# Optimization experiments

Hardware: AMD Instinct MI355X
Metric: run time of the kernel (lower is better)

Reference implementation:

```python
import jax, jax.numpy as jnp
import numpy as np

FREQ_DIM = 32
TIME_DIM = 32
HEADS = 8
TWO_PI = 6.283185307179586


def get_embeddings(B, H, W, freq_dim, time_dim, dtype):
    # freq embeddings over the height (frequency) axis
    nf = freq_dim // 2
    ln_x = jnp.log2(jnp.arange(0, H * nf, dtype=jnp.float32))
    ln_x = ln_x.at[0].set(-2.0)
    ln_x = ln_x.reshape(H, nf).T  # [nf, H]
    ln_x = ln_x * jnp.arange(1, nf + 1, dtype=jnp.float32)[:, None]
    # view_as_real(exp(1j*theta)) -> (cos, sin), interleaved per order along channel dim
    freq = jnp.stack([jnp.cos(ln_x), jnp.sin(ln_x)], axis=1).reshape(freq_dim, H)  # [freq_dim, H]
    freq = jnp.broadcast_to(freq[None, :, :, None], (B, freq_dim, H, W))

    # time embeddings over the width (time) axis
    nt = time_dim // 2
    k = jnp.arange(0, nt, dtype=jnp.float32) + 0.5  # [nt]
    x = jnp.arange(0, nt * W, dtype=jnp.float32).reshape(W, nt).T  # [nt, W]
    theta = k[:, None] * x / (W * nt) * TWO_PI  # [nt, W]
    time = jnp.stack([jnp.cos(theta), jnp.sin(theta)], axis=1).reshape(time_dim, W)  # [time_dim, W]
    time = jnp.broadcast_to(time[None, :, None, :], (B, time_dim, H, W))

    return jnp.concatenate([freq, time], axis=1).astype(dtype)  # [B, freq_dim+time_dim, H, W]


def setup_inputs() -> dict:
    key = jax.random.key(0)
    ks = jax.random.split(key, 6)
    B, C, H, W = 2, 512, 64, 32
    qkC = C + FREQ_DIM + TIME_DIM  # 576
    inner = HEADS * 64  # 512
    return {
        "hidden_states": jax.random.normal(ks[0], (B, C, H, W), dtype=jnp.float32),
        "Wq": jax.random.normal(ks[1], (qkC, inner), dtype=jnp.float32) * 0.02,
        "Wk": jax.random.normal(ks[2], (qkC, inner), dtype=jnp.float32) * 0.02,
        "Wv": jax.random.normal(ks[3], (C, inner), dtype=jnp.float32) * 0.02,
        "Wout": jax.random.normal(ks[4], (inner, C), dtype=jnp.float32) * 0.02,
        "bout": jnp.zeros((C,), dtype=jnp.float32),
    }


def reference(hidden_states, Wq, Wk, Wv, Wout, bout):
    B, C, H, W = hidden_states.shape
    emb = get_embeddings(B, H, W, FREQ_DIM, TIME_DIM, hidden_states.dtype)
    qk_hs = jnp.concatenate([hidden_states, emb], axis=1)  # [B, qkC, H, W]

    S = H * W
    qk_hs = qk_hs.reshape(B, -1, S).transpose(0, 2, 1)  # [B, S, qkC]
    v_hs = hidden_states.reshape(B, C, S).transpose(0, 2, 1)  # [B, S, C]

    q = qk_hs @ Wq  # [B, S, inner]
    k = qk_hs @ Wk
    v = v_hs @ Wv

    hd_qk = q.shape[-1] // HEADS
    hd_v = v.shape[-1] // HEADS
    q = q.reshape(B, S, HEADS, hd_qk).transpose(0, 2, 1, 3)  # [B, h, S, d]
    k = k.reshape(B, S, HEADS, hd_qk).transpose(0, 2, 1, 3)
    v = v.reshape(B, S, HEADS, hd_v).transpose(0, 2, 1, 3)

    scale = 1.0 / jnp.sqrt(jnp.asarray(hd_qk, dtype=q.dtype))
    scores = jnp.einsum('bhqd,bhkd->bhqk', q, k) * scale
    attn = jax.nn.softmax(scores, axis=-1)
    o = jnp.einsum('bhqk,bhkd->bhqd', attn, v)  # [B, h, S, d_v]

    o = o.transpose(0, 2, 1, 3).reshape(B, S, HEADS * hd_v)
    o = o @ Wout + bout  # [B, S, C]
    o = o.transpose(0, 2, 1).reshape(B, C, H, W)

    return o + hidden_states  # residual_connection=True, rescale_output_factor=1.0
```

## Files before the change

kernel.cpp:

```cpp
#include <hip/hip_runtime.h>
#include <math.h>

#define B_    2
#define C_    512
#define H_    64
#define W_    32
#define S_    2048
#define QKC_  576
#define INNER_ 512
#define NH_   8
#define HD_   64
#define TWO_PI_ 6.283185307179586f

typedef __attribute__((ext_vector_type(8))) short bfrag;
typedef __attribute__((ext_vector_type(4))) float ffrag;
typedef __attribute__((ext_vector_type(16))) float f16v;

typedef __attribute__((address_space(1))) const unsigned int as1_u32;
typedef __attribute__((address_space(3))) unsigned int as3_u32;

__device__ __forceinline__ ushort f2bf(float f) {
    unsigned u = __builtin_bit_cast(unsigned, f);
    unsigned r = (u + 0x7FFFu + ((u >> 16) & 1u)) >> 16;
    return (ushort)r;
}

__device__ __forceinline__ f16v zero16() {
    f16v z;
    #pragma unroll
    for (int i = 0; i < 16; i++) z[i] = 0.f;
    return z;
}

#define GLD(gp_, lp_) __builtin_amdgcn_global_load_lds((as1_u32*)(gp_), (as3_u32*)(lp_), 16, 0, 0)
#define EXPA(dst_, x_) asm("v_exp_f32 %0, %1" : "=v"(dst_) : "v"(x_))
#define SC_LOG2E 0.18033688011f

__global__ void k_trans_emb(const float* __restrict__ hid, ushort* __restrict__ X) {
    __shared__ float t[32][33];
    int b  = blockIdx.z;
    int s0 = blockIdx.x * 32, c0 = blockIdx.y * 32;
    int tx = threadIdx.x, ty = threadIdx.y;
    if (c0 < 512) {
        t[ty][tx] = hid[((size_t)b * C_ + (c0 + ty)) * S_ + s0 + tx];
        __syncthreads();
        X[((size_t)(b * S_ + s0 + ty)) * QKC_ + c0 + tx] = f2bf(t[tx][ty]);
    } else {
        int c = c0 - 512 + tx;
        int s = s0 + ty;
        int h = s >> 5, w = s & 31;
        float val;
        if (c < 32) {
            int f = c >> 1;
            int n = h * 16 + f;
            float lx = (n == 0) ? -2.0f : log2f((float)n);
            float arg = lx * (float)(f + 1);
            val = (c & 1) ? sinf(arg) : cosf(arg);
        } else {
            int tt = (c - 32) >> 1;
            float theta = ((float)tt + 0.5f) * (float)(w * 16 + tt) * (TWO_PI_ / 512.0f);
            val = (c & 1) ? sinf(theta) : cosf(theta);
        }
        X[(size_t)(b * S_ + s) * QKC_ + c0 + tx] = f2bf(val);
    }
}

__global__ void k_wtrans_all(const float* __restrict__ Wq, const float* __restrict__ Wk,
                             const float* __restrict__ Wv, const float* __restrict__ Wo,
                             ushort* __restrict__ Wqt, ushort* __restrict__ Wkt,
                             ushort* __restrict__ Wvt, ushort* __restrict__ Wot) {
    __shared__ float t[32][33];
    int z = blockIdx.z;
    const float* W; ushort* Wt; int K;
    if (z == 0)      { W = Wq; Wt = Wqt; K = QKC_; }
    else if (z == 1) { W = Wk; Wt = Wkt; K = QKC_; }
    else if (z == 2) { W = Wv; Wt = Wvt; K = C_; }
    else             { W = Wo; Wt = Wot; K = INNER_; }
    int k0 = blockIdx.x * 32, n0 = blockIdx.y * 32;
    if (k0 >= K) return;
    int tx = threadIdx.x, ty = threadIdx.y;
    t[ty][tx] = W[(size_t)(k0 + ty) * 512 + n0 + tx];
    __syncthreads();
    Wt[(size_t)(n0 + ty) * K + k0 + tx] = f2bf(t[tx][ty]);
}

#define GSTAGE(buf_, k0_) {                                                   \
    _Pragma("unroll")                                                         \
    for (int i_ = 0; i_ < 6; i_++)                                            \
        GLD(gp[i_] + (k0_), tl + (buf_) * 12288 + lo[i_]); }

__global__ __launch_bounds__(256, 3) void k_qkv(const ushort* __restrict__ X,
                                                const ushort* __restrict__ Wqt,
                                                const ushort* __restrict__ Wkt,
                                                const ushort* __restrict__ Wvt,
                                                ushort* __restrict__ Qb,
                                                ushort* __restrict__ Kpk,
                                                ushort* __restrict__ Vpk) {
    __shared__ ushort __attribute__((aligned(16))) tl[2 * 12288];

    int tid = threadIdx.x;
    int l = tid & 63, wv = tid >> 6;
    int wr = wv >> 1, wc = wv & 1;
    int bid = blockIdx.x;
    int lgc = (bid & 7) * 96 + (bid >> 3);
    int bx = lgc % 24, by = lgc / 24;
    int n0 = bx * 64, m0 = by * 128;
    int sel = n0 >> 9, n0l = n0 & 511;
    const ushort* Bt = (sel == 0) ? Wqt : (sel == 1) ? Wkt : Wvt;
    const int K = (sel < 2) ? QKC_ : C_;
    const int nst = K >> 6;
    int l15 = l & 15, lg = l >> 4;
    int swz = l15 & 7;

    const ushort* gp[6];
    unsigned lo[6];
    {
        int rsub = l >> 3;
        int clog = (l & 7) ^ rsub;
        #pragma unroll
        for (int i = 0; i < 6; i++) {
            int c = wv * 6 + i;
            lo[i] = c * 512;
            if (c < 16) gp[i] = X  + (size_t)(m0  + c * 8        + rsub) * QKC_ + clog * 8;
            else        gp[i] = Bt + (size_t)(n0l + (c - 16) * 8 + rsub) * K    + clog * 8;
        }
    }

    ffrag acc[4][2];
    #pragma unroll
    for (int i = 0; i < 4; i++)
        #pragma unroll
        for (int j = 0; j < 2; j++) acc[i][j] = (ffrag){0.f, 0.f, 0.f, 0.f};

    GSTAGE(0, 0);
    int cur = 0;
    for (int kt = 0; kt < nst; kt++) {
        __syncthreads();
        if (kt + 1 < nst) GSTAGE(cur ^ 1, (kt + 1) * 64);
        const ushort* As = tl + cur * 12288;
        const ushort* Bs = As + 8192;
        #pragma unroll
        for (int ks = 0; ks < 2; ks++) {
            int cl = ks * 4 + lg;
            int ch = (cl ^ swz) * 8;
            bfrag af[4], bf[2];
            #pragma unroll
            for (int mi = 0; mi < 4; mi++)
                af[mi] = *(const bfrag*)(As + (wr * 64 + mi * 16 + l15) * 64 + ch);
            #pragma unroll
            for (int nj = 0; nj < 2; nj++)
                bf[nj] = *(const bfrag*)(Bs + (wc * 32 + nj * 16 + l15) * 64 + ch);
            #pragma unroll
            for (int mi = 0; mi < 4; mi++)
                #pragma unroll
                for (int nj = 0; nj < 2; nj++)
                    acc[mi][nj] = __builtin_amdgcn_mfma_f32_16x16x32_bf16(af[mi], bf[nj], acc[mi][nj], 0, 0, 0);
        }
        cur ^= 1;
    }

    if (sel == 0) {
        #pragma unroll
        for (int mi = 0; mi < 4; mi++)
            #pragma unroll
            for (int nj = 0; nj < 2; nj++)
                #pragma unroll
                for (int r = 0; r < 4; r++) {
                    int row = m0 + wr * 64 + mi * 16 + lg * 4 + r;
                    int col = n0l + wc * 32 + nj * 16 + l15;
                    Qb[(size_t)row * INNER_ + col] = f2bf(acc[mi][nj][r] * SC_LOG2E);
                }
    } else {
        ushort (*Ct)[136] = (ushort(*)[136])tl;
        __syncthreads();
        #pragma unroll
        for (int mi = 0; mi < 4; mi++)
            #pragma unroll
            for (int nj = 0; nj < 2; nj++)
                #pragma unroll
                for (int r = 0; r < 4; r++)
                    Ct[wc * 32 + nj * 16 + l15][wr * 64 + mi * 16 + lg * 4 + r] = f2bf(acc[mi][nj][r]);
        __syncthreads();
        int pair = (m0 >> 11) * 8 + (n0l >> 6);
        int kvb0 = (m0 & 2047) >> 5;
        if (sel == 1) {
            #pragma unroll
            for (int p = 0; p < 4; p++) {
                int cid = tid + p * 256;
                int sl = cid >> 7, kv = cid & 127;
                bfrag tmp;
                #pragma unroll
                for (int j = 0; j < 8; j++) tmp[j] = (short)Ct[sl * 8 + j][kv];
                ushort* dst = Kpk + ((size_t)((pair * 64 + kvb0 + (kv >> 5)) * 8 + sl)) * 256 + (kv & 31) * 8;
                *(uint4*)dst = __builtin_bit_cast(uint4, tmp);
            }
        } else {
            #pragma unroll
            for (int p = 0; p < 4; p++) {
                int cid = tid + p * 256;
                int d = cid >> 4, mc = cid & 15;
                uint4 v = *(uint4*)&Ct[d][mc * 8];
                ushort* dst = Vpk + ((size_t)((pair * 64 + kvb0 + (mc >> 2)) * 4 + (mc & 3))) * 512 + d * 8;
                *(uint4*)dst = v;
            }
        }
    }
}

__global__ __launch_bounds__(256, 2) void k_og(const ushort* __restrict__ Ob,
                                               const ushort* __restrict__ Wot,
                                               const float* __restrict__ bias,
                                               const float* __restrict__ hid,
                                               float* __restrict__ out) {
    __shared__ ushort __attribute__((aligned(16))) tl[2 * 12288];

    int tid = threadIdx.x;
    int l = tid & 63, wv = tid >> 6;
    int wr = wv >> 1, wc = wv & 1;
    int bid = blockIdx.x;
    int lgc = (bid & 7) * 32 + (bid >> 3);
    int bx = lgc & 7, by = lgc >> 3;
    int n0 = bx * 64, m0 = by * 128;
    int l15 = l & 15, lg = l >> 4;
    int swz = l15 & 7;

    const ushort* gp[6];
    unsigned lo[6];
    {
        int rsub = l >> 3;
        int clog = (l & 7) ^ rsub;
        #pragma unroll
        for (int i = 0; i < 6; i++) {
            int c = wv * 6 + i;
            lo[i] = c * 512;
            if (c < 16) gp[i] = Ob  + (size_t)(m0 + c * 8        + rsub) * INNER_ + clog * 8;
            else        gp[i] = Wot + (size_t)(n0 + (c - 16) * 8 + rsub) * INNER_ + clog * 8;
        }
    }

    ffrag acc[4][2];
    #pragma unroll
    for (int i = 0; i < 4; i++)
        #pragma unroll
        for (int j = 0; j < 2; j++) acc[i][j] = (ffrag){0.f, 0.f, 0.f, 0.f};

    GSTAGE(0, 0);
    int cur = 0;
    for (int kt = 0; kt < 8; kt++) {
        __syncthreads();
        if (kt < 7) GSTAGE(cur ^ 1, (kt + 1) * 64);
        const ushort* As = tl + cur * 12288;
        const ushort* Bs = As + 8192;
        #pragma unroll
        for (int ks = 0; ks < 2; ks++) {
            int cl = ks * 4 + lg;
            int ch = (cl ^ swz) * 8;
            bfrag af[4], bf[2];
            #pragma unroll
            for (int mi = 0; mi < 4; mi++)
                af[mi] = *(const bfrag*)(As + (wr * 64 + mi * 16 + l15) * 64 + ch);
            #pragma unroll
            for (int nj = 0; nj < 2; nj++)
                bf[nj] = *(const bfrag*)(Bs + (wc * 32 + nj * 16 + l15) * 64 + ch);
            #pragma unroll
            for (int mi = 0; mi < 4; mi++)
                #pragma unroll
                for (int nj = 0; nj < 2; nj++)
                    acc[mi][nj] = __builtin_amdgcn_mfma_f32_16x16x32_bf16(af[mi], bf[nj], acc[mi][nj], 0, 0, 0);
        }
        cur ^= 1;
    }

    float (*Cf)[129] = (float(*)[129])tl;
    float bv[2];
    #pragma unroll
    for (int nj = 0; nj < 2; nj++) bv[nj] = bias[n0 + wc * 32 + nj * 16 + l15];
    __syncthreads();
    #pragma unroll
    for (int mi = 0; mi < 4; mi++)
        #pragma unroll
        for (int nj = 0; nj < 2; nj++)
            #pragma unroll
            for (int r = 0; r < 4; r++)
                Cf[wc * 32 + nj * 16 + l15][wr * 64 + mi * 16 + lg * 4 + r] = acc[mi][nj][r] + bv[nj];
    __syncthreads();
    int b = m0 >> 11, s0m = m0 & 2047;
    #pragma unroll
    for (int p = 0; p < 8; p++) {
        int f = p * 256 + tid;
        int c = f >> 5, sq = (f & 31) * 4;
        size_t o = (((size_t)(b * 512 + n0 + c)) << 11) + s0m + sq;
        float4 hv = *(const float4*)(hid + o);
        float4 cv = *(float4*)&Cf[c][sq];
        cv.x += hv.x; cv.y += hv.y; cv.z += hv.z; cv.w += hv.w;
        *(float4*)(out + o) = cv;
    }
}

#define CVTPK(dst, a, b) asm("v_cvt_pk_bf16_f32 %0, %1, %2" : "=v"(dst) : "v"(a), "v"(b))
#define SWAP32(a, b)     asm("v_permlane32_swap_b32 %0, %1" : "+v"(a), "+v"(b))

#define KLOAD(dst_, kt_) {                                                    \
    const ushort* g_ = kpb + (size_t)(kt_) * 2048 + kro;                      \
    _Pragma("unroll")                                                         \
    for (int ks_ = 0; ks_ < 4; ks_++) dst_[ks_] = *(const bfrag*)(g_ + ks_ * 512); }

#define VLOAD(dst_, kt_) {                                                    \
    const ushort* g_ = vpb + (size_t)(kt_) * 2048 + vro;                      \
    dst_[0] = *(const bfrag*)(g_);                                            \
    dst_[1] = *(const bfrag*)(g_ + 256);                                      \
    dst_[2] = *(const bfrag*)(g_ + 1024);                                     \
    dst_[3] = *(const bfrag*)(g_ + 1280); }

#define PVHALF(sf_, vf_, a0_, a1_) {                                          \
    _Pragma("unroll")                                                         \
    for (int s = 0; s < 2; s++) {                                             \
        unsigned A0, B0, A1, B1;                                              \
        CVTPK(A0, sf_[s * 8 + 0], sf_[s * 8 + 1]); CVTPK(B0, sf_[s * 8 + 4], sf_[s * 8 + 5]); \
        SWAP32(A0, B0);                                                       \
        CVTPK(A1, sf_[s * 8 + 2], sf_[s * 8 + 3]); CVTPK(B1, sf_[s * 8 + 6], sf_[s * 8 + 7]); \
        SWAP32(A1, B1);                                                       \
        uint4 u_; u_.x = A0; u_.y = A1; u_.z = B0; u_.w = B1;                 \
        bfrag pa_ = __builtin_bit_cast(bfrag, u_);                            \
        a0_ = __builtin_amdgcn_mfma_f32_32x32x16_bf16(vf_[s * 2],     pa_, a0_, 0, 0, 0); \
        a1_ = __builtin_amdgcn_mfma_f32_32x32x16_bf16(vf_[s * 2 + 1], pa_, a1_, 0, 0, 0); \
    } }

#define ABODY(kf_, vf_) {                                                     \
    f16v sfA = zero16(), sfB = zero16();                                      \
    __builtin_amdgcn_s_setprio(1);                                            \
    _Pragma("unroll")                                                         \
    for (int ks = 0; ks < 4; ks++) {                                          \
        sfA = __builtin_amdgcn_mfma_f32_32x32x16_bf16(kf_[ks], qfA[ks], sfA, 0, 0, 0); \
        sfB = __builtin_amdgcn_mfma_f32_32x32x16_bf16(kf_[ks], qfB[ks], sfB, 0, 0, 0); \
    }                                                                         \
    __builtin_amdgcn_s_setprio(0);                                            \
    float lsA = 0.f, lsB = 0.f;                                               \
    _Pragma("unroll")                                                         \
    for (int j = 0; j < 16; j++) {                                            \
        float pA; EXPA(pA, sfA[j]); sfA[j] = pA; lsA += pA;                   \
        float pB; EXPA(pB, sfB[j]); sfB[j] = pB; lsB += pB;                   \
    }                                                                         \
    lA += lsA; lB += lsB;                                                     \
    __builtin_amdgcn_s_setprio(1);                                            \
    PVHALF(sfA, vf_, accA0, accA1);                                           \
    PVHALF(sfB, vf_, accB0, accB1);                                           \
    __builtin_amdgcn_s_setprio(0); }

__global__ __launch_bounds__(512, 2) void k_attn(const ushort* __restrict__ Qf,
                                                 const ushort* __restrict__ Kpk,
                                                 const ushort* __restrict__ Vpk,
                                                 ushort* __restrict__ Ob) {
    __shared__ __attribute__((aligned(16))) char smem[35840];
    float* cmb = (float*)smem;
    float* lsh = (float*)(smem + 33792);

    const int id  = blockIdx.x;
    const int xcd = id & 7, wi = id >> 3;
    const int pair = xcd * 2 + (wi >> 4);
    const int qt   = wi & 15;
    const int hd = pair & 7, b = pair >> 3;

    const int tid = threadIdx.x;
    const int l = tid & 63, wvid = tid >> 6;
    const int qi = wvid >> 2, sp = wvid & 3;
    const int l31 = l & 31, hi = l >> 5;
    const int hoff = hd * HD_;
    const int brow = b * S_ + qt * 128;

    bfrag qfA[4], qfB[4];
    {
        const ushort* qpA = Qf + (size_t)(brow + qi * 64 + l31) * INNER_ + hoff + hi * 8;
        const ushort* qpB = qpA + (size_t)32 * INNER_;
        #pragma unroll
        for (int ks = 0; ks < 4; ks++) {
            qfA[ks] = *(const bfrag*)(qpA + ks * 16);
            qfB[ks] = *(const bfrag*)(qpB + ks * 16);
        }
    }

    const ushort* kpb = Kpk + ((size_t)pair * 64 + sp * 16) * 2048;
    const ushort* vpb = Vpk + ((size_t)pair * 64 + sp * 16) * 2048;
    const int kro = hi * 256 + l31 * 8;
    const int vro = hi * 512 + l31 * 8;

    float lA = 0.f, lB = 0.f;
    f16v accA0 = zero16(), accA1 = zero16();
    f16v accB0 = zero16(), accB1 = zero16();

    bfrag kc[4], vc[4], kn[4], vn[4];
    KLOAD(kc, 0); VLOAD(vc, 0);

    for (int it = 0; it < 16; it += 2) {
        if (it + 1 < 16) { KLOAD(kn, it + 1); VLOAD(vn, it + 1); }
        ABODY(kc, vc);
        if (it + 2 < 16) { KLOAD(kc, it + 2); VLOAD(vc, it + 2); }
        ABODY(kn, vn);
    }

    lA += __shfl_xor(lA, 32);
    lB += __shfl_xor(lB, 32);

    if (hi == 0) {
        lsh[((qi * 2 + 0) * 4 + sp) * 32 + l31] = lA;
        lsh[((qi * 2 + 1) * 4 + sp) * 32 + l31] = lB;
    }
    #pragma unroll
    for (int p = 0; p < 4; p++) {
        if (sp == p) {
            float* cA = cmb + (qi * 2 + 0) * 2112;
            float* cB = cmb + (qi * 2 + 1) * 2112;
            #pragma unroll
            for (int j = 0; j < 16; j++) {
                int d0 = (j & 3) + 8 * (j >> 2) + 4 * hi;
                if (p == 0) {
                    cA[d0 * 33 + l31]        = accA0[j];
                    cA[(d0 + 32) * 33 + l31] = accA1[j];
                    cB[d0 * 33 + l31]        = accB0[j];
                    cB[(d0 + 32) * 33 + l31] = accB1[j];
                } else {
                    cA[d0 * 33 + l31]        += accA0[j];
                    cA[(d0 + 32) * 33 + l31] += accA1[j];
                    cB[d0 * 33 + l31]        += accB0[j];
                    cB[(d0 + 32) * 33 + l31] += accB1[j];
                }
            }
        }
        __syncthreads();
    }
    #pragma unroll
    for (int p2 = 0; p2 < 2; p2++) {
        int f = p2 * 512 + tid;
        int qig = f >> 8;
        int t2 = f & 255;
        int qq = t2 >> 3, cc = t2 & 7;
        float lt = lsh[(qig * 4 + 0) * 32 + qq] + lsh[(qig * 4 + 1) * 32 + qq]
                 + lsh[(qig * 4 + 2) * 32 + qq] + lsh[(qig * 4 + 3) * 32 + qq];
        float inv = 1.0f / lt;
        bfrag ov;
        #pragma unroll
        for (int j = 0; j < 8; j++) {
            int d = cc * 8 + j;
            ov[j] = (short)f2bf(cmb[qig * 2112 + d * 33 + qq] * inv);
        }
        *(uint4*)(Ob + (size_t)(brow + qig * 32 + qq) * INNER_ + hoff + cc * 8) = __builtin_bit_cast(uint4, ov);
    }
}

extern "C" void kernel_launch(void* const* d_in, const int* in_sizes, int n_in,
                              void* d_out, int out_size, void* d_ws, size_t ws_size,
                              hipStream_t stream) {
    const float* hid  = (const float*)d_in[0];
    const float* Wq   = (const float*)d_in[1];
    const float* Wk   = (const float*)d_in[2];
    const float* Wv   = (const float*)d_in[3];
    const float* Wout = (const float*)d_in[4];
    const float* bout = (const float*)d_in[5];
    float* out = (float*)d_out;

    const int M = B_ * S_;
    char* w = (char*)d_ws;
    ushort* X    = (ushort*)w;                    w += (size_t)M * QKC_ * 2;
    ushort* Qb   = (ushort*)w;                    w += (size_t)M * INNER_ * 2;
    ushort* Kpk  = (ushort*)w;                    w += (size_t)M * INNER_ * 2;
    ushort* Vpk  = (ushort*)w;                    w += (size_t)M * INNER_ * 2;
    ushort* Ob   = (ushort*)w;                    w += (size_t)M * INNER_ * 2;
    ushort* Wqt  = (ushort*)w;                    w += (size_t)INNER_ * QKC_ * 2;
    ushort* Wkt  = (ushort*)w;                    w += (size_t)INNER_ * QKC_ * 2;
    ushort* Wvt  = (ushort*)w;                    w += (size_t)INNER_ * C_ * 2;
    ushort* Wot  = (ushort*)w;                    w += (size_t)C_ * INNER_ * 2;

    k_wtrans_all<<<dim3(18, 16, 4), dim3(32, 32), 0, stream>>>(Wq, Wk, Wv, Wout,
                                                               Wqt, Wkt, Wvt, Wot);
    k_trans_emb<<<dim3(S_ / 32, 18, B_), dim3(32, 32), 0, stream>>>(hid, X);

    k_qkv<<<dim3(768), 256, 0, stream>>>(X, Wqt, Wkt, Wvt, Qb, Kpk, Vpk);

    k_attn<<<dim3(256), 512, 0, stream>>>(Qb, Kpk, Vpk, Ob);

    k_og<<<dim3(256), 256, 0, stream>>>(Ob, Wot, bout, hid, out);
}
```

Before: 59.81 us.

## Merge prep kernels, parallelize softmax sums, and replace serialized split-K combine

The two preprocessing launches (weight transpose and activation transpose with embeddings) become one kernel with z selecting the role, which saves a launch. In the attention kernel the first QK MFMA now takes a zero constant directly, and the exp-sum uses four independent accumulators to shorten the dependency chain. The four serialized read-modify-write passes over shared memory, each followed by a barrier, are replaced by every wave writing its own partial accumulators to a much larger shared buffer (about 134 KB). The final pass then sums the four partials. The larger shared allocation may reduce blocks resident per CU below the launch-bounds target of two.

```diff
diff --git a/kernel.cpp b/kernel.cpp
--- a/kernel.cpp
+++ b/kernel.cpp
@@ -36,52 +36,54 @@
 #define EXPA(dst_, x_) asm("v_exp_f32 %0, %1" : "=v"(dst_) : "v"(x_))
 #define SC_LOG2E 0.18033688011f
 
-__global__ void k_trans_emb(const float* __restrict__ hid, ushort* __restrict__ X) {
+__global__ void k_pre(const float* __restrict__ hid,
+                      const float* __restrict__ Wq, const float* __restrict__ Wk,
+                      const float* __restrict__ Wv, const float* __restrict__ Wo,
+                      ushort* __restrict__ X,
+                      ushort* __restrict__ Wqt, ushort* __restrict__ Wkt,
+                      ushort* __restrict__ Wvt, ushort* __restrict__ Wot) {
     __shared__ float t[32][33];
-    int b  = blockIdx.z;
-    int s0 = blockIdx.x * 32, c0 = blockIdx.y * 32;
     int tx = threadIdx.x, ty = threadIdx.y;
-    if (c0 < 512) {
-        t[ty][tx] = hid[((size_t)b * C_ + (c0 + ty)) * S_ + s0 + tx];
+    int z = blockIdx.z;
+    if (z < 2) {
+        int b = z;
+        int s0 = blockIdx.x * 32, c0 = blockIdx.y * 32;
+        if (c0 < 512) {
+            t[ty][tx] = hid[((size_t)b * C_ + (c0 + ty)) * S_ + s0 + tx];
+            __syncthreads();
+            X[((size_t)(b * S_ + s0 + ty)) * QKC_ + c0 + tx] = f2bf(t[tx][ty]);
+        } else {
+            int c = c0 - 512 + tx;
+            int s = s0 + ty;
+            int h = s >> 5, w = s & 31;
+            float val;
+            if (c < 32) {
+                int f = c >> 1;
+                int n = h * 16 + f;
+                float lx = (n == 0) ? -2.0f : log2f((float)n);
+                float arg = lx * (float)(f + 1);
+                val = (c & 1) ? sinf(arg) : cosf(arg);
+            } else {
+                int tt = (c - 32) >> 1;
+                float theta = ((float)tt + 0.5f) * (float)(w * 16 + tt) * (TWO_PI_ / 512.0f);
+                val = (c & 1) ? sinf(theta) : cosf(theta);
+            }
+            X[(size_t)(b * S_ + s) * QKC_ + c0 + tx] = f2bf(val);
+        }
+    } else {
+        int idx = blockIdx.y * 64 + blockIdx.x;
+        int z4 = idx / 288, rem = idx % 288;
+        int k0 = (rem % 18) * 32, n0 = (rem / 18) * 32;
+        const float* W; ushort* Wt; int K;
+        if (z4 == 0)      { W = Wq; Wt = Wqt; K = QKC_; }
+        else if (z4 == 1) { W = Wk; Wt = Wkt; K = QKC_; }
+        else if (z4 == 2) { W = Wv; Wt = Wvt; K = C_; }
+        else              { W = Wo; Wt = Wot; K = INNER_; }
+        if (k0 >= K) return;
+        t[ty][tx] = W[(size_t)(k0 + ty) * 512 + n0 + tx];
         __syncthreads();
-        X[((size_t)(b * S_ + s0 + ty)) * QKC_ + c0 + tx] = f2bf(t[tx][ty]);
-    } else {
-        int c = c0 - 512 + tx;
-        int s = s0 + ty;
-        int h = s >> 5, w = s & 31;
-        float val;
-        if (c < 32) {
-            int f = c >> 1;
-            int n = h * 16 + f;
-            float lx = (n == 0) ? -2.0f : log2f((float)n);
-            float arg = lx * (float)(f + 1);
-            val = (c & 1) ? sinf(arg) : cosf(arg);
-        } else {
-            int tt = (c - 32) >> 1;
-            float theta = ((float)tt + 0.5f) * (float)(w * 16 + tt) * (TWO_PI_ / 512.0f);
-            val = (c & 1) ? sinf(theta) : cosf(theta);
-        }
-        X[(size_t)(b * S_ + s) * QKC_ + c0 + tx] = f2bf(val);
-    }
-}
-
-__global__ void k_wtrans_all(const float* __restrict__ Wq, const float* __restrict__ Wk,
-                             const float* __restrict__ Wv, const float* __restrict__ Wo,
-                             ushort* __restrict__ Wqt, ushort* __restrict__ Wkt,
-                             ushort* __restrict__ Wvt, ushort* __restrict__ Wot) {
-    __shared__ float t[32][33];
-    int z = blockIdx.z;
-    const float* W; ushort* Wt; int K;
-    if (z == 0)      { W = Wq; Wt = Wqt; K = QKC_; }
-    else if (z == 1) { W = Wk; Wt = Wkt; K = QKC_; }
-    else if (z == 2) { W = Wv; Wt = Wvt; K = C_; }
-    else             { W = Wo; Wt = Wot; K = INNER_; }
-    int k0 = blockIdx.x * 32, n0 = blockIdx.y * 32;
-    if (k0 >= K) return;
-    int tx = threadIdx.x, ty = threadIdx.y;
-    t[ty][tx] = W[(size_t)(k0 + ty) * 512 + n0 + tx];
-    __syncthreads();
-    Wt[(size_t)(n0 + ty) * K + k0 + tx] = f2bf(t[tx][ty]);
+        Wt[(size_t)(n0 + ty) * K + k0 + tx] = f2bf(t[tx][ty]);
+    }
 }
 
 #define GSTAGE(buf_, k0_) {                                                   \
@@ -327,21 +329,30 @@
     } }
 
 #define ABODY(kf_, vf_) {                                                     \
-    f16v sfA = zero16(), sfB = zero16();                                      \
     __builtin_amdgcn_s_setprio(1);                                            \
+    f16v sfA = __builtin_amdgcn_mfma_f32_32x32x16_bf16(kf_[0], qfA[0], fz, 0, 0, 0); \
+    f16v sfB = __builtin_amdgcn_mfma_f32_32x32x16_bf16(kf_[0], qfB[0], fz, 0, 0, 0); \
     _Pragma("unroll")                                                         \
-    for (int ks = 0; ks < 4; ks++) {                                          \
+    for (int ks = 1; ks < 4; ks++) {                                          \
         sfA = __builtin_amdgcn_mfma_f32_32x32x16_bf16(kf_[ks], qfA[ks], sfA, 0, 0, 0); \
         sfB = __builtin_amdgcn_mfma_f32_32x32x16_bf16(kf_[ks], qfB[ks], sfB, 0, 0, 0); \
     }                                                                         \
     __builtin_amdgcn_s_setprio(0);                                            \
-    float lsA = 0.f, lsB = 0.f;                                               \
+    float a0 = 0.f, a1 = 0.f, a2 = 0.f, a3 = 0.f;                             \
+    float b0 = 0.f, b1 = 0.f, b2 = 0.f, b3 = 0.f;                             \
     _Pragma("unroll")                                                         \
-    for (int j = 0; j < 16; j++) {                                            \
-        float pA; EXPA(pA, sfA[j]); sfA[j] = pA; lsA += pA;                   \
-        float pB; EXPA(pB, sfB[j]); sfB[j] = pB; lsB += pB;                   \
+    for (int j = 0; j < 4; j++) {                                             \
+        float pA0; EXPA(pA0, sfA[j]);      sfA[j] = pA0;      a0 += pA0;      \
+        float pA1; EXPA(pA1, sfA[j + 4]);  sfA[j + 4] = pA1;  a1 += pA1;      \
+        float pA2; EXPA(pA2, sfA[j + 8]);  sfA[j + 8] = pA2;  a2 += pA2;      \
+        float pA3; EXPA(pA3, sfA[j + 12]); sfA[j + 12] = pA3; a3 += pA3;      \
+        float pB0; EXPA(pB0, sfB[j]);      sfB[j] = pB0;      b0 += pB0;      \
+        float pB1; EXPA(pB1, sfB[j + 4]);  sfB[j + 4] = pB1;  b1 += pB1;      \
+        float pB2; EXPA(pB2, sfB[j + 8]);  sfB[j + 8] = pB2;  b2 += pB2;      \
+        float pB3; EXPA(pB3, sfB[j + 12]); sfB[j + 12] = pB3; b3 += pB3;      \
     }                                                                         \
-    lA += lsA; lB += lsB;                                                     \
+    lA += (a0 + a1) + (a2 + a3);                                              \
+    lB += (b0 + b1) + (b2 + b3);                                              \
     __builtin_amdgcn_s_setprio(1);                                            \
     PVHALF(sfA, vf_, accA0, accA1);                                           \
     PVHALF(sfB, vf_, accB0, accB1);                                           \
@@ -351,9 +362,9 @@
                                                  const ushort* __restrict__ Kpk,
                                                  const ushort* __restrict__ Vpk,
                                                  ushort* __restrict__ Ob) {
-    __shared__ __attribute__((aligned(16))) char smem[35840];
+    __shared__ __attribute__((aligned(16))) char smem[137216];
     float* cmb = (float*)smem;
-    float* lsh = (float*)(smem + 33792);
+    float* lsh = (float*)(smem + 135168);
 
     const int id  = blockIdx.x;
     const int xcd = id & 7, wi = id >> 3;
@@ -384,9 +395,10 @@
     const int kro = hi * 256 + l31 * 8;
     const int vro = hi * 512 + l31 * 8;
 
+    const f16v fz = zero16();
     float lA = 0.f, lB = 0.f;
-    f16v accA0 = zero16(), accA1 = zero16();
-    f16v accB0 = zero16(), accB1 = zero16();
+    f16v accA0 = fz, accA1 = fz;
+    f16v accB0 = fz, accB1 = fz;
 
     bfrag kc[4], vc[4], kn[4], vn[4];
     KLOAD(kc, 0); VLOAD(vc, 0);
@@ -402,46 +414,42 @@
     lB += __shfl_xor(lB, 32);
 
     if (hi == 0) {
-        lsh[((qi * 2 + 0) * 4 + sp) * 32 + l31] = lA;
-        lsh[((qi * 2 + 1) * 4 + sp) * 32 + l31] = lB;
-    }
-    #pragma unroll
-    for (int p = 0; p < 4; p++) {
-        if (sp == p) {
-            float* cA = cmb + (qi * 2 + 0) * 2112;
-            float* cB = cmb + (qi * 2 + 1) * 2112;
-            #pragma unroll
-            for (int j = 0; j < 16; j++) {
-                int d0 = (j & 3) + 8 * (j >> 2) + 4 * hi;
-                if (p == 0) {
-                    cA[d0 * 33 + l31]        = accA0[j];
-                    cA[(d0 + 32) * 33 + l31] = accA1[j];
-                    cB[d0 * 33 + l31]        = accB0[j];
-                    cB[(d0 + 32) * 33 + l31] = accB1[j];
-                } else {
-                    cA[d0 * 33 + l31]        += accA0[j];
-                    cA[(d0 + 32) * 33 + l31] += accA1[j];
-                    cB[d0 * 33 + l31]        += accB0[j];
-                    cB[(d0 + 32) * 33 + l31] += accB1[j];
-                }
-            }
-        }
-        __syncthreads();
-    }
+        lsh[(wvid * 2 + 0) * 32 + l31] = lA;
+        lsh[(wvid * 2 + 1) * 32 + l31] = lB;
+    }
+    {
+        float* cA = cmb + (wvid * 2 + 0) * 2112;
+        float* cB = cmb + (wvid * 2 + 1) * 2112;
+        #pragma unroll
+        for (int j = 0; j < 16; j++) {
+            int d0 = (j & 3) + 8 * (j >> 2) + 4 * hi;
+            cA[d0 * 33 + l31]        = accA0[j];
+            cA[(d0 + 32) * 33 + l31] = accA1[j];
+            cB[d0 * 33 + l31]        = accB0[j];
+            cB[(d0 + 32) * 33 + l31] = accB1[j];
+        }
+    }
+    __syncthreads();
     #pragma unroll
     for (int p2 = 0; p2 < 2; p2++) {
         int f = p2 * 512 + tid;
         int qig = f >> 8;
         int t2 = f & 255;
         int qq = t2 >> 3, cc = t2 & 7;
-        float lt = lsh[(qig * 4 + 0) * 32 + qq] + lsh[(qig * 4 + 1) * 32 + qq]
-                 + lsh[(qig * 4 + 2) * 32 + qq] + lsh[(qig * 4 + 3) * 32 + qq];
+        int qih = qig >> 1, g = qig & 1;
+        float lt = 0.f;
+        #pragma unroll
+        for (int s4 = 0; s4 < 4; s4++) lt += lsh[((qih * 4 + s4) * 2 + g) * 32 + qq];
         float inv = 1.0f / lt;
         bfrag ov;
         #pragma unroll
         for (int j = 0; j < 8; j++) {
             int d = cc * 8 + j;
-            ov[j] = (short)f2bf(cmb[qig * 2112 + d * 33 + qq] * inv);
+            float s = 0.f;
+            #pragma unroll
+            for (int s4 = 0; s4 < 4; s4++)
+                s += cmb[((qih * 4 + s4) * 2 + g) * 2112 + d * 33 + qq];
+            ov[j] = (short)f2bf(s * inv);
         }
         *(uint4*)(Ob + (size_t)(brow + qig * 32 + qq) * INNER_ + hoff + cc * 8) = __builtin_bit_cast(uint4, ov);
     }
@@ -470,9 +478,8 @@
     ushort* Wvt  = (ushort*)w;                    w += (size_t)INNER_ * C_ * 2;
     ushort* Wot  = (ushort*)w;                    w += (size_t)C_ * INNER_ * 2;
 
-    k_wtrans_all<<<dim3(18, 16, 4), dim3(32, 32), 0, stream>>>(Wq, Wk, Wv, Wout,
-                                                               Wqt, Wkt, Wvt, Wot);
-    k_trans_emb<<<dim3(S_ / 32, 18, B_), dim3(32, 32), 0, stream>>>(hid, X);
+    k_pre<<<dim3(64, 18, 3), dim3(32, 32), 0, stream>>>(hid, Wq, Wk, Wv, Wout,
+                                                        X, Wqt, Wkt, Wvt, Wot);
 
     k_qkv<<<dim3(768), 256, 0, stream>>>(X, Wqt, Wkt, Wvt, Qb, Kpk, Vpk);
 
```

New measurement: 56.26 us (median of 2 runs). -5.9%, faster.
